# Kernel tuning notes

Measured on AMD Instinct MI355X. Metric: run time of the kernel, lower is better.

## Reference

```python
import jax, jax.numpy as jnp
import numpy as np


def setup_inputs() -> dict:
    key = jax.random.key(0)
    ks = jax.random.split(key, 14)
    B, Ld, Lq, D = 64, 512, 128, 512
    d_node = jax.random.normal(ks[0], (B, Ld, D), jnp.float32)
    q_node = jax.random.normal(ks[1], (B, Lq, D), jnp.float32)
    qq_graph = jax.random.randint(ks[2], (B, Lq, Lq), 0, 2, jnp.int32)
    dq_graph = jax.random.randint(ks[3], (B, Ld, Lq), 0, 2, jnp.int32)
    dd_graph = jax.random.randint(ks[4], (B, Ld, Ld), 0, 2, jnp.int32)
    qd_graph = jax.random.randint(ks[5], (B, Lq, Ld), 0, 2, jnp.int32)
    s = 0.02
    W_nw = jax.random.normal(ks[6], (1, D), jnp.float32) * s
    b_nw = jnp.zeros((1,), jnp.float32)
    W_self = jax.random.normal(ks[7], (D, D), jnp.float32) * s
    b_self = jnp.zeros((D,), jnp.float32)
    W_dd = jax.random.normal(ks[8], (D, D), jnp.float32) * s
    W_qq = jax.random.normal(ks[9], (D, D), jnp.float32) * s
    W_dq = jax.random.normal(ks[10], (D, D), jnp.float32) * s
    W_qd = jax.random.normal(ks[11], (D, D), jnp.float32) * s
    return {"d_node": d_node, "q_node": q_node, "qq_graph": qq_graph,
            "dq_graph": dq_graph, "dd_graph": dd_graph, "qd_graph": qd_graph,
            "W_nw": W_nw, "b_nw": b_nw, "W_self": W_self, "b_self": b_self,
            "W_dd": W_dd, "W_qq": W_qq, "W_dq": W_dq, "W_qd": W_qd,
            "iteration_steps": 2}


def reference(d_node, q_node, qq_graph, dq_graph, dd_graph, qd_graph,
              W_nw, b_nw, W_self, b_self, W_dd, W_qq, W_dq, W_qd,
              iteration_steps):
    dd = dd_graph.astype(jnp.float32)
    dq = dq_graph.astype(jnp.float32)
    qq = qq_graph.astype(jnp.float32)
    qd = qd_graph.astype(jnp.float32)

    # neighbor counts, clamped to 1 where a node has no neighbors
    d_nb = dd.sum(-1) + dq.sum(-1)              # [B, Ld]
    d_nb = jnp.where(d_nb >= 1.0, d_nb, 1.0)
    q_nb = qq.sum(-1) + qd.sum(-1)              # [B, Lq]
    q_nb = jnp.where(q_nb >= 1.0, q_nb, 1.0)

    all_d_w, all_q_w = [], []
    for _ in range(iteration_steps):
        d_w = jax.nn.sigmoid(jnp.einsum('bld,od->blo', d_node, W_nw) + b_nw)[..., 0]  # [B, Ld]
        q_w = jax.nn.sigmoid(jnp.einsum('bld,od->blo', q_node, W_nw) + b_nw)[..., 0]  # [B, Lq]
        all_d_w.append(d_w)
        all_q_w.append(q_w)

        self_d = jnp.einsum('bld,od->blo', d_node, W_self) + b_self
        self_q = jnp.einsum('bld,od->blo', q_node, W_self) + b_self
        dd_info = jnp.einsum('bld,od->blo', d_node, W_dd)
        qd_info = jnp.einsum('bld,od->blo', d_node, W_qd)
        qq_info = jnp.einsum('bld,od->blo', q_node, W_qq)
        dq_info = jnp.einsum('bld,od->blo', q_node, W_dq)

        # masked weights: graph is 0/1, so replace_masked_values(., graph, 0) == graph * weight
        dd_msg = jnp.einsum('bij,bjd->bid', dd * d_w[:, None, :], dd_info)  # [B,Ld,D]
        qd_msg = jnp.einsum('bij,bjd->bid', qd * d_w[:, None, :], qd_info)  # [B,Lq,D]
        qq_msg = jnp.einsum('bij,bjd->bid', qq * q_w[:, None, :], qq_info)  # [B,Lq,D]
        dq_msg = jnp.einsum('bij,bjd->bid', dq * q_w[:, None, :], dq_info)  # [B,Ld,D]

        agg_q = (qq_msg + qd_msg) / q_nb[..., None]
        agg_d = (dd_msg + dq_msg) / d_nb[..., None]
        d_node = jax.nn.relu(self_d + agg_d)
        q_node = jax.nn.relu(self_q + agg_q)

    all_d_w = jnp.stack(all_d_w, axis=1)  # [B, steps, Ld]
    all_q_w = jnp.stack(all_q_w, axis=1)  # [B, steps, Lq]
    return (d_node, q_node, all_d_w, all_q_w)
```

## Files before the change

kernel.cpp:

```cpp
#include <hip/hip_runtime.h>
#include <cstdint>
#include <cstddef>

typedef _Float16 h16;
typedef __attribute__((ext_vector_type(8))) _Float16 h16x8;
typedef __attribute__((ext_vector_type(4))) _Float16 h16x4;
typedef __attribute__((ext_vector_type(4))) float f32x4;

constexpr int B_ = 64, LD = 512, LQ = 128, DIM = 512, STEPS = 2;
constexpr int MD = B_ * LD;
constexpr int MQ = B_ * LQ;
constexpr int KST = LD + LQ;
constexpr int KAGG = KST + DIM;

struct Src {
  const h16* p0; int s0; long bstr0;
  const h16* p1; int s1; long bstr1;
  int ksplit;
};

template <class Epi>
__global__ __launch_bounds__(256) void gemm2(Src sa, Src sb, int K, Epi epi) {
  const int b = blockIdx.z;

  __shared__ __align__(16) h16 lds[2 * 2 * 4096];

  const int tid = threadIdx.x;
  const int lane = tid & 63;
  const int wv = tid >> 6;
  const int wm = (wv >> 1) * 64, wn = (wv & 1) * 64;
  const int quad = lane >> 4, l16 = lane & 15;
  const long tileM = (long)blockIdx.x * 128, tileN = (long)blockIdx.y * 128;
  const int r = tid >> 2;
  const int kq = tid & 3;

  const h16* pa0 = sa.p0 + (size_t)b * sa.bstr0 + (tileM + r) * (long)sa.s0 + kq * 8;
  const h16* pa0h = pa0 + 64L * sa.s0;
  const h16* pa1 = sa.p1 + (size_t)b * sa.bstr1 + (tileM + r) * (long)sa.s1 + kq * 8 - sa.ksplit;
  const h16* pa1h = pa1 + 64L * sa.s1;
  const h16* pb0 = sb.p0 + (size_t)b * sb.bstr0 + (tileN + r) * (long)sb.s0 + kq * 8;
  const h16* pb0h = pb0 + 64L * sb.s0;
  const h16* pb1 = sb.p1 + (size_t)b * sb.bstr1 + (tileN + r) * (long)sb.s1 + kq * 8 - sb.ksplit;
  const h16* pb1h = pb1 + 64L * sb.s1;

  const int pw = (kq * 128 + (r ^ (2 * kq))) * 8;
  h16* const dA = &lds[pw];
  h16* const dB = &lds[4096 + pw];

  const h16* fA[4];
  const h16* fB[4];
#pragma unroll
  for (int t = 0; t < 4; t++) {
    const int rowA = wm + t * 16 + l16;
    const int rowB = wn + t * 16 + l16;
    fA[t] = &lds[(quad * 128 + (rowA ^ (2 * quad))) * 8];
    fB[t] = &lds[4096 + (quad * 128 + (rowB ^ (2 * quad))) * 8];
  }

  f32x4 acc[4][4] = {};
  const int T = K >> 5;

  h16x8 ra0, ra1, rb0, rb1;
  auto loadT = [&](int t) {
    const int k0 = t * 32;
    const bool fa = k0 < sa.ksplit;
    ra0 = *(const h16x8*)((fa ? pa0 : pa1) + k0);
    ra1 = *(const h16x8*)((fa ? pa0h : pa1h) + k0);
    const bool fb = k0 < sb.ksplit;
    rb0 = *(const h16x8*)((fb ? pb0 : pb1) + k0);
    rb1 = *(const h16x8*)((fb ? pb0h : pb1h) + k0);
  };

  loadT(0);
  *(h16x8*)dA = ra0;
  *(h16x8*)(dA + 64 * 8) = ra1;
  *(h16x8*)dB = rb0;
  *(h16x8*)(dB + 64 * 8) = rb1;
  loadT(1);

  auto step = [&](int t, int c) {
    __syncthreads();
    h16x8 af[4], bf[4];
    const int off = c * 8192;
#pragma unroll
    for (int i = 0; i < 4; i++) {
      af[i] = *(const h16x8*)(fA[i] + off);
      bf[i] = *(const h16x8*)(fB[i] + off);
    }
    if (t + 1 < T) {
      const int o2 = (c ^ 1) * 8192;
      *(h16x8*)(dA + o2) = ra0;
      *(h16x8*)(dA + o2 + 64 * 8) = ra1;
      *(h16x8*)(dB + o2) = rb0;
      *(h16x8*)(dB + o2 + 64 * 8) = rb1;
    }
    if (t + 2 < T) loadT(t + 2);
#pragma unroll
    for (int i = 0; i < 4; i++)
#pragma unroll
      for (int j = 0; j < 4; j++)
        acc[i][j] = __builtin_amdgcn_mfma_f32_16x16x32_f16(af[i], bf[j], acc[i][j], 0, 0, 0);
  };

  for (int t = 0; t < T; t += 2) {
    step(t, 0);
    step(t + 1, 1);
  }

#pragma unroll
  for (int i = 0; i < 4; i++) {
#pragma unroll
    for (int j = 0; j < 4; j++) {
      const int gm0 = (int)tileM + wm + i * 16 + quad * 4;
      const int gn  = (int)tileN + wn + j * 16 + l16;
#pragma unroll
      for (int rr = 0; rr < 4; rr++) epi(b, gm0 + rr, gn, acc[i][j][rr]);
    }
  }
}

struct EpiDense {
  const float* w;
  h16* stackA;
  h16* stackB;
  int lnShift;
  int offA, offB;
  __device__ void operator()(int, int gm, int gn, float v) const {
    const int b = gn >> lnShift, l = gn & ((1 << lnShift) - 1);
    const h16 sv = (h16)(w[gn] * v);
    if (gm < 512)
      stackA[((size_t)b * 512 + gm) * 640 + offA + l] = sv;
    else
      stackB[((size_t)b * 512 + (gm - 512)) * 640 + offB + l] = sv;
  }
};
struct EpiAgg {
  const float* bias;
  float* out;
  h16* nodeNext;
  int rowsPerB;
  __device__ void operator()(int b, int gm, int gn, float v) const {
    const size_t row = (size_t)b * rowsPerB + gm;
    const float val = fmaxf(v + bias[gn], 0.f);
    if (out) out[row * 512 + gn] = val;
    nodeNext[row * 512 + gn] = (h16)val;
  }
};

__global__ __launch_bounds__(256) void k_convert(const float* __restrict__ dn,
                                                 const float* __restrict__ qn,
                                                 h16* __restrict__ dnb,
                                                 h16* __restrict__ qnb) {
  const size_t i4 = ((size_t)blockIdx.x * 256 + threadIdx.x) * 4;
  constexpr size_t TD = (size_t)MD * DIM;
  const float* src; h16* dst; size_t idx;
  if (i4 < TD) { src = dn; dst = dnb; idx = i4; }
  else         { src = qn; dst = qnb; idx = i4 - TD; }
  const float4 v = *(const float4*)&src[idx];
  h16x4 o; o.x = (h16)v.x; o.y = (h16)v.y; o.z = (h16)v.z; o.w = (h16)v.w;
  *(h16x4*)&dst[idx] = o;
}

__global__ __launch_bounds__(256) void k_wcat(const float* __restrict__ Wself,
                                              const float* __restrict__ Wdd,
                                              const float* __restrict__ Wqd,
                                              const float* __restrict__ Wqq,
                                              const float* __restrict__ Wdq,
                                              h16* __restrict__ catD,
                                              h16* __restrict__ catQ) {
  const int i = blockIdx.x * 256 + threadIdx.x;
  float vD, vQ;
  if (i < 512 * 512)       { vD = Wself[i];            vQ = vD; }
  else if (i < 1024 * 512) { vD = Wdd[i - 512 * 512];  vQ = Wqq[i - 512 * 512]; }
  else                     { vD = Wqd[i - 1024 * 512]; vQ = Wdq[i - 1024 * 512]; }
  catD[i] = (h16)vD; catQ[i] = (h16)vQ;
}

__global__ __launch_bounds__(256) void k_maskD(const int* __restrict__ dd,
                                               const int* __restrict__ dq,
                                               h16* __restrict__ maskD) {
  const int row = blockIdx.x * 4 + (threadIdx.x >> 6);
  const int lane = threadIdx.x & 63;
  const int* pdd = dd + (size_t)row * 512;
  const int* pdq = dq + (size_t)row * 128;
  h16* pm = maskD + (size_t)row * 640;
  float vals[10];
  float s = 0.f;
#pragma unroll
  for (int t = 0; t < 10; t++) {
    const int j = lane + t * 64;
    const float v = (float)((j < 512) ? pdd[j] : pdq[j - 512]);
    vals[t] = v; s += v;
  }
  for (int m = 32; m; m >>= 1) s += __shfl_xor(s, m);
  const float inv = 1.f / fmaxf(s, 1.f);
#pragma unroll
  for (int t = 0; t < 10; t++) pm[lane + t * 64] = (h16)(vals[t] * inv);
}

__global__ __launch_bounds__(256) void k_maskQ(const int* __restrict__ qq,
                                               const int* __restrict__ qd,
                                               h16* __restrict__ maskQ) {
  const int row = blockIdx.x * 4 + (threadIdx.x >> 6);
  const int lane = threadIdx.x & 63;
  const int* pqq = qq + (size_t)row * 128;
  const int* pqd = qd + (size_t)row * 512;
  h16* pm = maskQ + (size_t)row * 640;
  float vals[10];
  float s = 0.f;
#pragma unroll
  for (int t = 0; t < 10; t++) {
    const int j = lane + t * 64;
    const float v = (float)((j < 128) ? pqq[j] : pqd[j - 128]);
    vals[t] = v; s += v;
  }
  for (int m = 32; m; m >>= 1) s += __shfl_xor(s, m);
  const float inv = 1.f / fmaxf(s, 1.f);
#pragma unroll
  for (int t = 0; t < 10; t++) pm[lane + t * 64] = (h16)(vals[t] * inv);
}

__global__ __launch_bounds__(256) void k_w(const h16* __restrict__ dnb,
                                           const h16* __restrict__ qnb,
                                           const float* __restrict__ Wnw,
                                           const float* __restrict__ bnw,
                                           float* __restrict__ d_w,
                                           float* __restrict__ q_w,
                                           float* __restrict__ adw,
                                           float* __restrict__ aqw, int it) {
  const int row = blockIdx.x * 4 + (threadIdx.x >> 6);
  const int lane = threadIdx.x & 63;
  const bool isD = row < MD;
  const h16* node = isD ? dnb + (size_t)row * 512 : qnb + (size_t)(row - MD) * 512;
  const h16x8 v = *(const h16x8*)&node[lane * 8];
  const float4 w0 = *(const float4*)&Wnw[lane * 8];
  const float4 w1 = *(const float4*)&Wnw[lane * 8 + 4];
  float s = (float)v[0] * w0.x + (float)v[1] * w0.y + (float)v[2] * w0.z +
            (float)v[3] * w0.w + (float)v[4] * w1.x + (float)v[5] * w1.y +
            (float)v[6] * w1.z + (float)v[7] * w1.w;
  for (int m = 32; m; m >>= 1) s += __shfl_xor(s, m);
  if (lane == 0) {
    const float w = 1.f / (1.f + expf(-(s + bnw[0])));
    if (isD) {
      d_w[row] = w;
      adw[((size_t)(row >> 9) * STEPS + it) * 512 + (row & 511)] = w;
    } else {
      const int rq = row - MD;
      q_w[rq] = w;
      aqw[((size_t)(rq >> 7) * STEPS + it) * 128 + (rq & 127)] = w;
    }
  }
}

extern "C" void kernel_launch(void* const* d_in, const int* in_sizes, int n_in,
                              void* d_out, int out_size, void* d_ws, size_t ws_size,
                              hipStream_t stream) {
  (void)in_sizes; (void)n_in; (void)out_size; (void)ws_size;

  const float* d_node = (const float*)d_in[0];
  const float* q_node = (const float*)d_in[1];
  const int*   qq     = (const int*)d_in[2];
  const int*   dq     = (const int*)d_in[3];
  const int*   dd     = (const int*)d_in[4];
  const int*   qd     = (const int*)d_in[5];
  const float* W_nw   = (const float*)d_in[6];
  const float* b_nw   = (const float*)d_in[7];
  const float* W_self = (const float*)d_in[8];
  const float* b_self = (const float*)d_in[9];
  const float* W_dd   = (const float*)d_in[10];
  const float* W_qq   = (const float*)d_in[11];
  const float* W_dq   = (const float*)d_in[12];
  const float* W_qd   = (const float*)d_in[13];

  float* outd = (float*)d_out;
  float* outq = outd + (size_t)MD * DIM;
  float* adw  = outq + (size_t)MQ * DIM;
  float* aqw  = adw + (size_t)B_ * STEPS * LD;

  char* p = (char*)d_ws;
  auto alloc = [&](size_t bytes) { char* r = p; p += (bytes + 255) & ~(size_t)255; return r; };
  h16* dnode[2], *qnode[2];
  dnode[0] = (h16*)alloc((size_t)MD * DIM * 2);
  dnode[1] = (h16*)alloc((size_t)MD * DIM * 2);
  qnode[0] = (h16*)alloc((size_t)MQ * DIM * 2);
  qnode[1] = (h16*)alloc((size_t)MQ * DIM * 2);
  h16* catD    = (h16*)alloc((size_t)1536 * 512 * 2);
  h16* catQ    = (h16*)alloc((size_t)1536 * 512 * 2);
  h16* maskD   = (h16*)alloc((size_t)B_ * LD * KST * 2);
  h16* maskQ   = (h16*)alloc((size_t)B_ * LQ * KST * 2);
  h16* stackDT = (h16*)alloc((size_t)B_ * 512 * KST * 2);
  h16* stackQT = (h16*)alloc((size_t)B_ * 512 * KST * 2);
  float* d_wb  = (float*)alloc((size_t)MD * 4);
  float* q_wb  = (float*)alloc((size_t)MQ * 4);

  k_convert<<<dim3((MD * DIM + MQ * DIM) / 4 / 256), 256, 0, stream>>>(d_node, q_node, dnode[0], qnode[0]);
  k_wcat<<<dim3(1536 * 512 / 256), 256, 0, stream>>>(W_self, W_dd, W_qd, W_qq, W_dq, catD, catQ);
  k_maskD<<<dim3(MD / 4), 256, 0, stream>>>(dd, dq, maskD);
  k_maskQ<<<dim3(MQ / 4), 256, 0, stream>>>(qq, qd, maskQ);

  for (int it = 0; it < STEPS; it++) {
    const bool last = (it == STEPS - 1);
    h16* ncur_d = dnode[it & 1];
    h16* nnext_d = dnode[(it & 1) ^ 1];
    h16* ncur_q = qnode[it & 1];
    h16* nnext_q = qnode[(it & 1) ^ 1];

    k_w<<<dim3((MD + MQ) / 4), 256, 0, stream>>>(ncur_d, ncur_q, W_nw, b_nw, d_wb, q_wb, adw, aqw, it);

    {
      Src sa{catD + 512 * 512, 512, 0, catD + 512 * 512, 512, 0, 512};
      Src sb{ncur_d, 512, 0, ncur_d, 512, 0, 512};
      gemm2<<<dim3(1024 / 128, MD / 128, 1), 256, 0, stream>>>(
          sa, sb, 512, EpiDense{d_wb, stackDT, stackQT, 9, 0, 128});
    }
    {
      Src sa{catQ + 512 * 512, 512, 0, catQ + 512 * 512, 512, 0, 512};
      Src sb{ncur_q, 512, 0, ncur_q, 512, 0, 512};
      gemm2<<<dim3(1024 / 128, MQ / 128, 1), 256, 0, stream>>>(
          sa, sb, 512, EpiDense{q_wb, stackQT, stackDT, 7, 0, 512});
    }
    {
      Src sa{maskD, 640, (long)LD * KST, ncur_d, 512, (long)LD * DIM, KST};
      Src sb{stackDT, 640, (long)512 * KST, catD, 512, 0, KST};
      gemm2<<<dim3(LD / 128, 512 / 128, B_), 256, 0, stream>>>(
          sa, sb, KAGG, EpiAgg{b_self, last ? outd : nullptr, nnext_d, 512});
    }
    {
      Src sa{maskQ, 640, (long)LQ * KST, ncur_q, 512, (long)LQ * DIM, KST};
      Src sb{stackQT, 640, (long)512 * KST, catQ, 512, 0, KST};
      gemm2<<<dim3(LQ / 128, 512 / 128, B_), 256, 0, stream>>>(
          sa, sb, KAGG, EpiAgg{b_self, last ? outq : nullptr, nnext_q, 128});
    }
  }
}
```

Measured before the change: 657.4 us.

## Merge D/Q GEMM launches into combined kernels and deepen global prefetch

Combines the separate D and Q dense-projection GEMMs into one launch, and likewise the two aggregation GEMMs, with the block index dispatching to the D or Q problem. This removes two launches per iteration and lets the small Q work fill idle CUs alongside the D tiles. The GEMM main loop now keeps two register staging sets and prefetches global tiles two steps ahead, hiding more load latency at the cost of extra VGPRs and possible lower occupancy. The block-to-tile mapping also changes, which may alter cache reuse.

```diff
diff --git a/kernel.cpp b/kernel.cpp
--- a/kernel.cpp
+++ b/kernel.cpp
@@ -20,17 +20,14 @@
 };
 
 template <class Epi>
-__global__ __launch_bounds__(256) void gemm2(Src sa, Src sb, int K, Epi epi) {
-  const int b = blockIdx.z;
-
-  __shared__ __align__(16) h16 lds[2 * 2 * 4096];
-
+__device__ __forceinline__ void gemm_body(int b, long tileM, long tileN,
+                                          Src sa, Src sb, int K,
+                                          const Epi& epi, h16* lds) {
   const int tid = threadIdx.x;
   const int lane = tid & 63;
   const int wv = tid >> 6;
   const int wm = (wv >> 1) * 64, wn = (wv & 1) * 64;
   const int quad = lane >> 4, l16 = lane & 15;
-  const long tileM = (long)blockIdx.x * 128, tileN = (long)blockIdx.y * 128;
   const int r = tid >> 2;
   const int kq = tid & 3;
 
@@ -60,41 +57,30 @@
   f32x4 acc[4][4] = {};
   const int T = K >> 5;
 
-  h16x8 ra0, ra1, rb0, rb1;
-  auto loadT = [&](int t) {
+  h16x8 s0[4], s1[4];
+  auto loadInto = [&](h16x8* s, int t) {
     const int k0 = t * 32;
     const bool fa = k0 < sa.ksplit;
-    ra0 = *(const h16x8*)((fa ? pa0 : pa1) + k0);
-    ra1 = *(const h16x8*)((fa ? pa0h : pa1h) + k0);
+    s[0] = *(const h16x8*)((fa ? pa0 : pa1) + k0);
+    s[1] = *(const h16x8*)((fa ? pa0h : pa1h) + k0);
     const bool fb = k0 < sb.ksplit;
-    rb0 = *(const h16x8*)((fb ? pb0 : pb1) + k0);
-    rb1 = *(const h16x8*)((fb ? pb0h : pb1h) + k0);
+    s[2] = *(const h16x8*)((fb ? pb0 : pb1) + k0);
+    s[3] = *(const h16x8*)((fb ? pb0h : pb1h) + k0);
   };
-
-  loadT(0);
-  *(h16x8*)dA = ra0;
-  *(h16x8*)(dA + 64 * 8) = ra1;
-  *(h16x8*)dB = rb0;
-  *(h16x8*)(dB + 64 * 8) = rb1;
-  loadT(1);
-
-  auto step = [&](int t, int c) {
-    __syncthreads();
+  auto writeLDS = [&](const h16x8* s, int c) {
+    const int o = c * 8192;
+    *(h16x8*)(dA + o) = s[0];
+    *(h16x8*)(dA + o + 512) = s[1];
+    *(h16x8*)(dB + o) = s[2];
+    *(h16x8*)(dB + o + 512) = s[3];
+  };
+  auto mfma16 = [&](const int off) {
     h16x8 af[4], bf[4];
-    const int off = c * 8192;
 #pragma unroll
     for (int i = 0; i < 4; i++) {
       af[i] = *(const h16x8*)(fA[i] + off);
       bf[i] = *(const h16x8*)(fB[i] + off);
     }
-    if (t + 1 < T) {
-      const int o2 = (c ^ 1) * 8192;
-      *(h16x8*)(dA + o2) = ra0;
-      *(h16x8*)(dA + o2 + 64 * 8) = ra1;
-      *(h16x8*)(dB + o2) = rb0;
-      *(h16x8*)(dB + o2 + 64 * 8) = rb1;
-    }
-    if (t + 2 < T) loadT(t + 2);
 #pragma unroll
     for (int i = 0; i < 4; i++)
 #pragma unroll
@@ -102,9 +88,38 @@
         acc[i][j] = __builtin_amdgcn_mfma_f32_16x16x32_f16(af[i], bf[j], acc[i][j], 0, 0, 0);
   };
 
+  loadInto(s0, 0);
+  writeLDS(s0, 0);
+  loadInto(s0, 1);
+  if (2 < T) loadInto(s1, 2);
+
   for (int t = 0; t < T; t += 2) {
-    step(t, 0);
-    step(t + 1, 1);
+    __syncthreads();
+    {
+      h16x8 af[4], bf[4];
+#pragma unroll
+      for (int i = 0; i < 4; i++) { af[i] = *(const h16x8*)fA[i]; bf[i] = *(const h16x8*)fB[i]; }
+      writeLDS(s0, 1);
+      if (t + 3 < T) loadInto(s0, t + 3);
+#pragma unroll
+      for (int i = 0; i < 4; i++)
+#pragma unroll
+        for (int j = 0; j < 4; j++)
+          acc[i][j] = __builtin_amdgcn_mfma_f32_16x16x32_f16(af[i], bf[j], acc[i][j], 0, 0, 0);
+    }
+    __syncthreads();
+    {
+      h16x8 af[4], bf[4];
+#pragma unroll
+      for (int i = 0; i < 4; i++) { af[i] = *(const h16x8*)(fA[i] + 8192); bf[i] = *(const h16x8*)(fB[i] + 8192); }
+      if (t + 2 < T) writeLDS(s1, 0);
+      if (t + 4 < T) loadInto(s1, t + 4);
+#pragma unroll
+      for (int i = 0; i < 4; i++)
+#pragma unroll
+        for (int j = 0; j < 4; j++)
+          acc[i][j] = __builtin_amdgcn_mfma_f32_16x16x32_f16(af[i], bf[j], acc[i][j], 0, 0, 0);
+    }
   }
 
 #pragma unroll
@@ -146,6 +161,30 @@
     nodeNext[row * 512 + gn] = (h16)val;
   }
 };
+
+__global__ __launch_bounds__(256) void k_dense(Src saD, Src sbD, EpiDense epiD,
+                                               Src saQ, Src sbQ, EpiDense epiQ) {
+  __shared__ __align__(16) h16 lds[2 * 2 * 4096];
+  const int g = blockIdx.x;
+  const int x = g / 320;
+  const int yy = g % 320;
+  if (yy < 256)
+    gemm_body(0, (long)x * 128, (long)yy * 128, saD, sbD, 512, epiD, lds);
+  else
+    gemm_body(0, (long)x * 128, (long)(yy - 256) * 128, saQ, sbQ, 512, epiQ, lds);
+}
+
+__global__ __launch_bounds__(256) void k_agg(Src saD, Src sbD, EpiAgg epiD,
+                                             Src saQ, Src sbQ, EpiAgg epiQ) {
+  __shared__ __align__(16) h16 lds[2 * 2 * 4096];
+  const int g = blockIdx.x;
+  const int b = g & 63;
+  const int inner = g >> 6;
+  if (inner < 16)
+    gemm_body(b, (long)(inner >> 2) * 128, (long)(inner & 3) * 128, saD, sbD, KAGG, epiD, lds);
+  else
+    gemm_body(b, 0L, (long)(inner - 16) * 128, saQ, sbQ, KAGG, epiQ, lds);
+}
 
 __global__ __launch_bounds__(256) void k_convert(const float* __restrict__ dn,
                                                  const float* __restrict__ qn,
@@ -308,28 +347,22 @@
     k_w<<<dim3((MD + MQ) / 4), 256, 0, stream>>>(ncur_d, ncur_q, W_nw, b_nw, d_wb, q_wb, adw, aqw, it);
 
     {
-      Src sa{catD + 512 * 512, 512, 0, catD + 512 * 512, 512, 0, 512};
-      Src sb{ncur_d, 512, 0, ncur_d, 512, 0, 512};
-      gemm2<<<dim3(1024 / 128, MD / 128, 1), 256, 0, stream>>>(
-          sa, sb, 512, EpiDense{d_wb, stackDT, stackQT, 9, 0, 128});
+      Src saD{catD + 512 * 512, 512, 0, catD + 512 * 512, 512, 0, 512};
+      Src sbD{ncur_d, 512, 0, ncur_d, 512, 0, 512};
+      Src saQ{catQ + 512 * 512, 512, 0, catQ + 512 * 512, 512, 0, 512};
+      Src sbQ{ncur_q, 512, 0, ncur_q, 512, 0, 512};
+      k_dense<<<dim3(2560), 256, 0, stream>>>(
+          saD, sbD, EpiDense{d_wb, stackDT, stackQT, 9, 0, 128},
+          saQ, sbQ, EpiDense{q_wb, stackQT, stackDT, 7, 0, 512});
     }
     {
-      Src sa{catQ + 512 * 512, 512, 0, catQ + 512 * 512, 512, 0, 512};
-      Src sb{ncur_q, 512, 0, ncur_q, 512, 0, 512};
-      gemm2<<<dim3(1024 / 128, MQ / 128, 1), 256, 0, stream>>>(
-          sa, sb, 512, EpiDense{q_wb, stackQT, stackDT, 7, 0, 512});
-    }
-    {
-      Src sa{maskD, 640, (long)LD * KST, ncur_d, 512, (long)LD * DIM, KST};
-      Src sb{stackDT, 640, (long)512 * KST, catD, 512, 0, KST};
-      gemm2<<<dim3(LD / 128, 512 / 128, B_), 256, 0, stream>>>(
-          sa, sb, KAGG, EpiAgg{b_self, last ? outd : nullptr, nnext_d, 512});
-    }
-    {
-      Src sa{maskQ, 640, (long)LQ * KST, ncur_q, 512, (long)LQ * DIM, KST};
-      Src sb{stackQT, 640, (long)512 * KST, catQ, 512, 0, KST};
-      gemm2<<<dim3(LQ / 128, 512 / 128, B_), 256, 0, stream>>>(
-          sa, sb, KAGG, EpiAgg{b_self, last ? outq : nullptr, nnext_q, 128});
-    }
-  }
-}
+      Src saD{maskD, 640, (long)LD * KST, ncur_d, 512, (long)LD * DIM, KST};
+      Src sbD{stackDT, 640, (long)512 * KST, catD, 512, 0, KST};
+      Src saQ{maskQ, 640, (long)LQ * KST, ncur_q, 512, (long)LQ * DIM, KST};
+      Src sbQ{stackQT, 640, (long)512 * KST, catQ, 512, 0, KST};
+      k_agg<<<dim3(1280), 256, 0, stream>>>(
+          saD, sbD, EpiAgg{b_self, last ? outd : nullptr, nnext_d, 512},
+          saQ, sbQ, EpiAgg{b_self, last ? outq : nullptr, nnext_q, 128});
+    }
+  }
+}
```

Result: faster. 627.1 us (-4.6%).
